# Kernel optimization log

Hardware: AMD Instinct MI355X
Metric: run time of the kernel (lower is better)

Reference implementation:

```python
import jax, jax.numpy as jnp
import numpy as np
import math

CEN_W = 1.0
ANG_W = 1.0


def _radius(ndim):
    # Iterative version of the recursive Radius() from the source.
    if ndim < 1:
        raise ValueError('ndim >= 1 required')
    if ndim == 1:
        return 0.0
    r = 0.5
    for _ in range(3, ndim + 1):
        r = 0.5 / math.sqrt(1.0 - r * r)
    return r


def _costheta(ndim):
    return 2.0 * _radius(ndim - 1) ** 2 - 1.0


def setup_inputs() -> dict:
    key = jax.random.key(0)
    k1, k2, k3 = jax.random.split(key, 3)
    B, C, D = 65536, 1000, 512
    y = jax.random.randint(k1, (B,), 0, C, dtype=jnp.int64 if jax.config.jax_enable_x64 else jnp.int32)
    feat = jax.random.normal(k2, (B, D), dtype=jnp.float32)
    centers = jax.random.normal(k3, (C, D), dtype=jnp.float32)
    return {"y": y, "feat": feat, "centers": centers}


def reference(y, feat, centers):
    C = centers.shape[0]
    B = feat.shape[0]
    ct = jnp.float32(_costheta(C))  # static Python constant from num_classes

    # ---- center loss: gather assigned centers, squared diff sum ----
    centers_pred = centers[y]                      # [B, D] gather
    diff = feat - centers_pred
    loss_cen = 0.5 * jnp.sum(diff * diff) / B

    # ---- angular loss: vectorized Gram matrix over classes ----
    # In torch, centers[j].data and dist are detached -> stop_gradient here.
    centers_sg = jax.lax.stop_gradient(centers)
    dist = jnp.linalg.norm(centers_sg, axis=1)     # [C], detached
    gram = centers @ centers_sg.T                  # [C, C]; grad flows via rows only
    sim = gram / (dist[:, None] * dist[None, :])
    offdiag = 1.0 - jnp.eye(C, dtype=sim.dtype)
    loss_ang = jnp.sum(offdiag * (sim - ct) ** 2) / (0.5 * C * (C - 1))

    return loss_cen * CEN_W + loss_ang * ANG_W
```

## Files before the change

### kernel.cpp

```cpp
#include <hip/hip_runtime.h>
#include <math.h>

typedef __attribute__((ext_vector_type(8))) short bf16x8;
typedef __attribute__((ext_vector_type(4))) float f32x4;
typedef __attribute__((ext_vector_type(4))) float vf4;

__device__ __forceinline__ float wave_reduce(float v) {
#pragma unroll
    for (int off = 32; off > 0; off >>= 1) v += __shfl_down(v, off, 64);
    return v;
}

__device__ __forceinline__ unsigned short f2bf(float x) {
    unsigned u = __float_as_uint(x);
    u += 0x7FFFu + ((u >> 16) & 1u);
    return (unsigned short)(u >> 16);
}

__global__ __launch_bounds__(128) void prep_kernel(const float4* __restrict__ cent4,
                                                   ushort4* __restrict__ xb,
                                                   float* __restrict__ dist2,
                                                   float* __restrict__ out,
                                                   int C, int d4) {
    const int r = blockIdx.x;
    const int t = threadIdx.x;
    if (r == 0 && t == 0) out[0] = 0.f;
    __shared__ float sm[2];
    float s = 0.f;
    for (int c = t; c < d4; c += blockDim.x) {
        float4 f = make_float4(0.f, 0.f, 0.f, 0.f);
        if (r < C) f = cent4[(size_t)r * d4 + c];
        s += f.x * f.x + f.y * f.y + f.z * f.z + f.w * f.w;
        ushort4 h;
        h.x = f2bf(f.x); h.y = f2bf(f.y); h.z = f2bf(f.z); h.w = f2bf(f.w);
        xb[(size_t)r * d4 + c] = h;
    }
    s = wave_reduce(s);
    const int lane = t & 63, w = t >> 6;
    if (lane == 0) sm[w] = s;
    __syncthreads();
    if (t == 0) {
        float tot = sm[0];
        if (blockDim.x > 64) tot += sm[1];
        dist2[r] = (r < C) ? tot : 1.0f;
    }
}

__global__ __launch_bounds__(256) void fused_kernel(const int* __restrict__ y,
                                                    const vf4* __restrict__ feat4,
                                                    const float4* __restrict__ cent4,
                                                    const unsigned short* __restrict__ xb,
                                                    const float* __restrict__ dist2,
                                                    float* __restrict__ out,
                                                    int n4, int d4, float cen_scale,
                                                    int C, int D, int ntile,
                                                    float ct, float ang_scale,
                                                    int ang_blocks, int center_blocks) {
    __shared__ float sm[4];
    const int lane = threadIdx.x & 63;
    const int wid = threadIdx.x >> 6;

    if ((int)blockIdx.x < ang_blocks) {
        const int w = blockIdx.x * 4 + wid;
        float local = 0.f;
        if (w < ntile * ntile) {
            const int ti = w / ntile;
            const int tj = w - ti * ntile;
            const int n = lane & 15;
            const int quad = lane >> 4;
            const int dv = D >> 3;
            const bf16x8* ap = (const bf16x8*)xb + (size_t)(ti * 16 + n) * dv + quad;
            const bf16x8* bp = (const bf16x8*)xb + (size_t)(tj * 16 + n) * dv + quad;
            f32x4 acc = {0.f, 0.f, 0.f, 0.f};
            const int steps = D >> 5;
#pragma unroll 8
            for (int st = 0; st < steps; ++st) {
                bf16x8 a = ap[st * 4];
                bf16x8 b = bp[st * 4];
                acc = __builtin_amdgcn_mfma_f32_16x16x32_bf16(a, b, acc, 0, 0, 0);
            }
            const int gj = tj * 16 + n;
            const float dj = dist2[gj];
#pragma unroll
            for (int rr = 0; rr < 4; ++rr) {
                const int gi = ti * 16 + quad * 4 + rr;
                if (gi < C && gj < C && gi != gj) {
                    float sim = acc[rr] * rsqrtf(dist2[gi] * dj);
                    float dlt = sim - ct;
                    local += dlt * dlt;
                }
            }
        }
        local = wave_reduce(local);
        if (lane == 0) sm[wid] = local;
        __syncthreads();
        if (threadIdx.x == 0) {
            float tot = sm[0] + sm[1] + sm[2] + sm[3];
            atomicAdd(out, tot * ang_scale);
        }
    } else {
        const int cb = blockIdx.x - ang_blocks;
        const int stride = center_blocks * 256;
        float s = 0.f;
        int i = cb * 256 + threadIdx.x;
        if ((stride % d4) == 0) {
            if (i < n4) {
                int row = i / d4;
                const int col = i - row * d4;
                const int rstep = stride / d4;
                for (; i < n4; i += stride, row += rstep) {
                    const int cls = y[row];
                    vf4 f = __builtin_nontemporal_load(feat4 + i);
                    float4 c = cent4[(size_t)cls * d4 + col];
                    float dx = f.x - c.x, dy = f.y - c.y, dz = f.z - c.z, dw = f.w - c.w;
                    s += dx * dx + dy * dy + dz * dz + dw * dw;
                }
            }
        } else {
            for (; i < n4; i += stride) {
                int row = i / d4;
                int col = i - row * d4;
                const int cls = y[row];
                vf4 f = __builtin_nontemporal_load(feat4 + i);
                float4 c = cent4[(size_t)cls * d4 + col];
                float dx = f.x - c.x, dy = f.y - c.y, dz = f.z - c.z, dw = f.w - c.w;
                s += dx * dx + dy * dy + dz * dz + dw * dw;
            }
        }
        s = wave_reduce(s);
        if (lane == 0) sm[wid] = s;
        __syncthreads();
        if (threadIdx.x == 0) {
            float tot = sm[0] + sm[1] + sm[2] + sm[3];
            atomicAdd(out, tot * cen_scale);
        }
    }
}

extern "C" void kernel_launch(void* const* d_in, const int* in_sizes, int n_in,
                              void* d_out, int out_size, void* d_ws, size_t ws_size,
                              hipStream_t stream) {
    const int* y = (const int*)d_in[0];
    const float* feat = (const float*)d_in[1];
    const float* centers = (const float*)d_in[2];

    const int B = in_sizes[0];
    const int D = in_sizes[1] / B;
    const int C = in_sizes[2] / D;
    const int d4 = D / 4;
    const int ntile = (C + 15) / 16;
    const int Cpad = ntile * 16;

    const int nd = C - 1;
    double r = 0.0;
    if (nd >= 2) {
        r = 0.5;
        for (int i = 3; i <= nd; ++i) r = 0.5 / sqrt(1.0 - r * r);
    }
    const float ct = (float)(2.0 * r * r - 1.0);

    float* outp = (float*)d_out;
    char* ws = (char*)d_ws;
    unsigned short* xb = (unsigned short*)ws;
    size_t xb_bytes = (size_t)Cpad * D * sizeof(unsigned short);
    float* dist2 = (float*)(ws + ((xb_bytes + 255) & ~(size_t)255));

    prep_kernel<<<Cpad, 128, 0, stream>>>((const float4*)centers, (ushort4*)xb, dist2,
                                          outp, C, d4);

    const int n4 = B * d4;
    const float cen_scale = (float)(0.5 / (double)B);
    const float ang_scale = (float)(1.0 / (0.5 * (double)C * (double)(C - 1)));
    const int ntile2 = ntile * ntile;
    const int ang_blocks = (ntile2 + 3) / 4;
    const int center_blocks = 2048;

    fused_kernel<<<ang_blocks + center_blocks, 256, 0, stream>>>(
        y, (const vf4*)feat, (const float4*)centers, xb, dist2, outp,
        n4, d4, cen_scale, C, D, ntile, ct, ang_scale, ang_blocks, center_blocks);
}
```

Baseline: 224.5 us.

## Merge prep and fused kernels into one cooperative persistent kernel with grid sync

Removes the separate bf16-conversion/norm prep kernel. Centers are now read as fp32 in the Gram loop, converted to bf16 on the fly, and squared norms are computed inline with shuffles. Everything runs in a single cooperative launch sized by occupancy, with a persistent grid-stride schedule. Per-block partials are reduced by block 0 after a grid sync, replacing the atomics. This trades one launch and the workspace round-trip for redundant fp32 loads and conversions in the angular tiles, plus a grid barrier.

```diff
diff --git a/kernel.cpp b/kernel.cpp
--- a/kernel.cpp
+++ b/kernel.cpp
@@ -1,5 +1,8 @@
 #include <hip/hip_runtime.h>
+#include <hip/hip_cooperative_groups.h>
 #include <math.h>
+
+namespace cg = cooperative_groups;
 
 typedef __attribute__((ext_vector_type(8))) short bf16x8;
 typedef __attribute__((ext_vector_type(4))) float f32x4;
@@ -17,123 +20,127 @@
     return (unsigned short)(u >> 16);
 }
 
-__global__ __launch_bounds__(128) void prep_kernel(const float4* __restrict__ cent4,
-                                                   ushort4* __restrict__ xb,
-                                                   float* __restrict__ dist2,
-                                                   float* __restrict__ out,
-                                                   int C, int d4) {
-    const int r = blockIdx.x;
-    const int t = threadIdx.x;
-    if (r == 0 && t == 0) out[0] = 0.f;
-    __shared__ float sm[2];
-    float s = 0.f;
-    for (int c = t; c < d4; c += blockDim.x) {
-        float4 f = make_float4(0.f, 0.f, 0.f, 0.f);
-        if (r < C) f = cent4[(size_t)r * d4 + c];
-        s += f.x * f.x + f.y * f.y + f.z * f.z + f.w * f.w;
-        ushort4 h;
-        h.x = f2bf(f.x); h.y = f2bf(f.y); h.z = f2bf(f.z); h.w = f2bf(f.w);
-        xb[(size_t)r * d4 + c] = h;
-    }
-    s = wave_reduce(s);
-    const int lane = t & 63, w = t >> 6;
-    if (lane == 0) sm[w] = s;
-    __syncthreads();
-    if (t == 0) {
-        float tot = sm[0];
-        if (blockDim.x > 64) tot += sm[1];
-        dist2[r] = (r < C) ? tot : 1.0f;
-    }
-}
+struct Params {
+    const int* y;
+    const vf4* feat4;
+    const vf4* cent4;
+    float* partials;
+    float* out;
+    int n4, d4, C, ntile, steps, ang_blocks;
+    float cen_scale, ang_scale, ct;
+};
 
-__global__ __launch_bounds__(256) void fused_kernel(const int* __restrict__ y,
-                                                    const vf4* __restrict__ feat4,
-                                                    const float4* __restrict__ cent4,
-                                                    const unsigned short* __restrict__ xb,
-                                                    const float* __restrict__ dist2,
-                                                    float* __restrict__ out,
-                                                    int n4, int d4, float cen_scale,
-                                                    int C, int D, int ntile,
-                                                    float ct, float ang_scale,
-                                                    int ang_blocks, int center_blocks) {
-    __shared__ float sm[4];
+__global__ __launch_bounds__(256) void one_kernel(Params p) {
+    const int bid = blockIdx.x;
+    const int nb = gridDim.x;
     const int lane = threadIdx.x & 63;
     const int wid = threadIdx.x >> 6;
+    __shared__ float sm[4];
 
-    if ((int)blockIdx.x < ang_blocks) {
-        const int w = blockIdx.x * 4 + wid;
+    float partial = 0.f;
+
+    if (bid < p.ang_blocks) {
+        const int wglob = bid * 4 + wid;
+        const int wstride = p.ang_blocks * 4;
+        const int n = lane & 15;
+        const int quad = lane >> 4;
+        const int ntile2 = p.ntile * p.ntile;
         float local = 0.f;
-        if (w < ntile * ntile) {
-            const int ti = w / ntile;
-            const int tj = w - ti * ntile;
-            const int n = lane & 15;
-            const int quad = lane >> 4;
-            const int dv = D >> 3;
-            const bf16x8* ap = (const bf16x8*)xb + (size_t)(ti * 16 + n) * dv + quad;
-            const bf16x8* bp = (const bf16x8*)xb + (size_t)(tj * 16 + n) * dv + quad;
+        for (int t = wglob; t < ntile2; t += wstride) {
+            const int ti = t / p.ntile;
+            const int tj = t - ti * p.ntile;
+            const int ra = ti * 16 + n;
+            const int rb = tj * 16 + n;
+            const bool va = ra < p.C;
+            const bool vb = rb < p.C;
+            const vf4* aptr = p.cent4 + (size_t)ra * p.d4 + quad * 2;
+            const vf4* bptr = p.cent4 + (size_t)rb * p.d4 + quad * 2;
             f32x4 acc = {0.f, 0.f, 0.f, 0.f};
-            const int steps = D >> 5;
-#pragma unroll 8
-            for (int st = 0; st < steps; ++st) {
-                bf16x8 a = ap[st * 4];
-                bf16x8 b = bp[st * 4];
-                acc = __builtin_amdgcn_mfma_f32_16x16x32_bf16(a, b, acc, 0, 0, 0);
+            float sa = 0.f, sb = 0.f;
+#pragma unroll 4
+            for (int st = 0; st < p.steps; ++st) {
+                vf4 a0 = {0.f, 0.f, 0.f, 0.f}, a1 = a0, b0 = a0, b1 = a0;
+                if (va) { a0 = aptr[st * 8]; a1 = aptr[st * 8 + 1]; }
+                if (vb) { b0 = bptr[st * 8]; b1 = bptr[st * 8 + 1]; }
+                sa += a0.x * a0.x + a0.y * a0.y + a0.z * a0.z + a0.w * a0.w
+                    + a1.x * a1.x + a1.y * a1.y + a1.z * a1.z + a1.w * a1.w;
+                sb += b0.x * b0.x + b0.y * b0.y + b0.z * b0.z + b0.w * b0.w
+                    + b1.x * b1.x + b1.y * b1.y + b1.z * b1.z + b1.w * b1.w;
+                bf16x8 af, bf;
+                af[0] = (short)f2bf(a0.x); af[1] = (short)f2bf(a0.y);
+                af[2] = (short)f2bf(a0.z); af[3] = (short)f2bf(a0.w);
+                af[4] = (short)f2bf(a1.x); af[5] = (short)f2bf(a1.y);
+                af[6] = (short)f2bf(a1.z); af[7] = (short)f2bf(a1.w);
+                bf[0] = (short)f2bf(b0.x); bf[1] = (short)f2bf(b0.y);
+                bf[2] = (short)f2bf(b0.z); bf[3] = (short)f2bf(b0.w);
+                bf[4] = (short)f2bf(b1.x); bf[5] = (short)f2bf(b1.y);
+                bf[6] = (short)f2bf(b1.z); bf[7] = (short)f2bf(b1.w);
+                acc = __builtin_amdgcn_mfma_f32_16x16x32_bf16(af, bf, acc, 0, 0, 0);
             }
+            sa += __shfl_xor(sa, 16, 64); sa += __shfl_xor(sa, 32, 64);
+            sb += __shfl_xor(sb, 16, 64); sb += __shfl_xor(sb, 32, 64);
+            float di[4];
+#pragma unroll
+            for (int rr = 0; rr < 4; ++rr) di[rr] = __shfl(sa, quad * 4 + rr, 64);
             const int gj = tj * 16 + n;
-            const float dj = dist2[gj];
+            const float dj = sb;
 #pragma unroll
             for (int rr = 0; rr < 4; ++rr) {
                 const int gi = ti * 16 + quad * 4 + rr;
-                if (gi < C && gj < C && gi != gj) {
-                    float sim = acc[rr] * rsqrtf(dist2[gi] * dj);
-                    float dlt = sim - ct;
+                if (gi < p.C && gj < p.C && gi != gj) {
+                    float sim = acc[rr] * rsqrtf(di[rr] * dj);
+                    float dlt = sim - p.ct;
                     local += dlt * dlt;
                 }
             }
         }
-        local = wave_reduce(local);
-        if (lane == 0) sm[wid] = local;
-        __syncthreads();
-        if (threadIdx.x == 0) {
-            float tot = sm[0] + sm[1] + sm[2] + sm[3];
-            atomicAdd(out, tot * ang_scale);
-        }
+        partial = local * p.ang_scale;
     } else {
-        const int cb = blockIdx.x - ang_blocks;
-        const int stride = center_blocks * 256;
+        const int cb = bid - p.ang_blocks;
+        const int stride = (nb - p.ang_blocks) * 256;
         float s = 0.f;
         int i = cb * 256 + threadIdx.x;
-        if ((stride % d4) == 0) {
-            if (i < n4) {
-                int row = i / d4;
-                const int col = i - row * d4;
-                const int rstep = stride / d4;
-                for (; i < n4; i += stride, row += rstep) {
-                    const int cls = y[row];
-                    vf4 f = __builtin_nontemporal_load(feat4 + i);
-                    float4 c = cent4[(size_t)cls * d4 + col];
+        if ((stride % p.d4) == 0) {
+            if (i < p.n4) {
+                int row = i / p.d4;
+                const int col = i - row * p.d4;
+                const int rstep = stride / p.d4;
+                for (; i < p.n4; i += stride, row += rstep) {
+                    const int cls = p.y[row];
+                    vf4 f = __builtin_nontemporal_load(p.feat4 + i);
+                    vf4 c = p.cent4[(size_t)cls * p.d4 + col];
                     float dx = f.x - c.x, dy = f.y - c.y, dz = f.z - c.z, dw = f.w - c.w;
                     s += dx * dx + dy * dy + dz * dz + dw * dw;
                 }
             }
         } else {
-            for (; i < n4; i += stride) {
-                int row = i / d4;
-                int col = i - row * d4;
-                const int cls = y[row];
-                vf4 f = __builtin_nontemporal_load(feat4 + i);
-                float4 c = cent4[(size_t)cls * d4 + col];
+            for (; i < p.n4; i += stride) {
+                int row = i / p.d4;
+                int col = i - row * p.d4;
+                const int cls = p.y[row];
+                vf4 f = __builtin_nontemporal_load(p.feat4 + i);
+                vf4 c = p.cent4[(size_t)cls * p.d4 + col];
                 float dx = f.x - c.x, dy = f.y - c.y, dz = f.z - c.z, dw = f.w - c.w;
                 s += dx * dx + dy * dy + dz * dz + dw * dw;
             }
         }
+        partial = s * p.cen_scale;
+    }
+
+    float r = wave_reduce(partial);
+    if (lane == 0) sm[wid] = r;
+    __syncthreads();
+    if (threadIdx.x == 0) p.partials[bid] = sm[0] + sm[1] + sm[2] + sm[3];
+
+    cg::this_grid().sync();
+
+    if (bid == 0) {
+        float s = 0.f;
+        for (int i = threadIdx.x; i < nb; i += 256) s += p.partials[i];
         s = wave_reduce(s);
         if (lane == 0) sm[wid] = s;
         __syncthreads();
-        if (threadIdx.x == 0) {
-            float tot = sm[0] + sm[1] + sm[2] + sm[3];
-            atomicAdd(out, tot * cen_scale);
-        }
+        if (threadIdx.x == 0) p.out[0] = sm[0] + sm[1] + sm[2] + sm[3];
     }
 }
 
@@ -149,7 +156,6 @@
     const int C = in_sizes[2] / D;
     const int d4 = D / 4;
     const int ntile = (C + 15) / 16;
-    const int Cpad = ntile * 16;
 
     const int nd = C - 1;
     double r = 0.0;
@@ -159,23 +165,30 @@
     }
     const float ct = (float)(2.0 * r * r - 1.0);
 
-    float* outp = (float*)d_out;
-    char* ws = (char*)d_ws;
-    unsigned short* xb = (unsigned short*)ws;
-    size_t xb_bytes = (size_t)Cpad * D * sizeof(unsigned short);
-    float* dist2 = (float*)(ws + ((xb_bytes + 255) & ~(size_t)255));
+    int maxB = 0;
+    if (hipOccupancyMaxActiveBlocksPerMultiprocessor(&maxB, one_kernel, 256, 0) != hipSuccess
+        || maxB < 1) maxB = 4;
+    int grid = maxB * 256;
+    if (grid > 2048) grid = 2048;
+    const int ang_blocks = grid / 8;
 
-    prep_kernel<<<Cpad, 128, 0, stream>>>((const float4*)centers, (ushort4*)xb, dist2,
-                                          outp, C, d4);
+    Params p;
+    p.y = y;
+    p.feat4 = (const vf4*)feat;
+    p.cent4 = (const vf4*)centers;
+    p.partials = (float*)d_ws;
+    p.out = (float*)d_out;
+    p.n4 = B * d4;
+    p.d4 = d4;
+    p.C = C;
+    p.ntile = ntile;
+    p.steps = D / 32;
+    p.ang_blocks = ang_blocks;
+    p.cen_scale = (float)(0.5 / (double)B);
+    p.ang_scale = (float)(1.0 / (0.5 * (double)C * (double)(C - 1)));
+    p.ct = ct;
 
-    const int n4 = B * d4;
-    const float cen_scale = (float)(0.5 / (double)B);
-    const float ang_scale = (float)(1.0 / (0.5 * (double)C * (double)(C - 1)));
-    const int ntile2 = ntile * ntile;
-    const int ang_blocks = (ntile2 + 3) / 4;
-    const int center_blocks = 2048;
-
-    fused_kernel<<<ang_blocks + center_blocks, 256, 0, stream>>>(
-        y, (const vf4*)feat, (const float4*)centers, xb, dist2, outp,
-        n4, d4, cen_scale, C, D, ntile, ct, ang_scale, ang_blocks, center_blocks);
+    void* args[] = { &p };
+    hipLaunchCooperativeKernel((const void*)one_kernel, dim3(grid), dim3(256),
+                               args, 0, stream);
 }
```

Result: slower. 402.1 us (+79.1%).
